# Optimization experiments

Hardware: AMD Instinct MI355X
Metric: run time of the kernel (lower is better)

Reference implementation:

```python
import jax, jax.numpy as jnp
import numpy as np

TOP_K = 2


def setup_inputs() -> dict:
    key = jax.random.key(0)
    ks = jax.random.split(key, 5)
    B, S, D, F, E = 2, 2048, 1024, 3584, 8
    scale_in = 1.0 / np.sqrt(D)
    scale_f = 1.0 / np.sqrt(F)
    return {
        "hidden_states": jax.random.normal(ks[0], (B, S, D), dtype=jnp.float32),
        "gate_w": jax.random.normal(ks[1], (E, D), dtype=jnp.float32) * scale_in,
        "w1": jax.random.normal(ks[2], (E, F, D), dtype=jnp.float32) * scale_in,
        "w3": jax.random.normal(ks[3], (E, F, D), dtype=jnp.float32) * scale_in,
        "w2": jax.random.normal(ks[4], (E, D, F), dtype=jnp.float32) * scale_f,
    }


def _routing_weights(logits):
    # softmax over experts, select top-k, renormalize (Mixtral semantics)
    probs = jax.nn.softmax(logits, axis=-1)          # [T, E]
    topv, topi = jax.lax.top_k(probs, TOP_K)          # [T, k]
    topv = topv / jnp.sum(topv, axis=-1, keepdims=True)
    T, E = logits.shape
    w = jnp.zeros((T, E), dtype=logits.dtype)
    w = w.at[jnp.arange(T)[:, None], topi].set(topv)  # dense [T, E] routing weights
    return w


def reference(hidden_states, gate_w, w1, w3, w2):
    B, S, D = hidden_states.shape
    x = hidden_states.reshape(-1, D)                  # [T, D]
    logits = x @ gate_w.T                             # [T, E]
    rw = _routing_weights(logits)                     # [T, E]
    E = gate_w.shape[0]
    out = jnp.zeros_like(x)
    for e in range(E):                                # fixed small expert count
        h = jax.nn.silu(x @ w1[e].T) * (x @ w3[e].T)  # [T, F]
        out = out + rw[:, e:e + 1] * (h @ w2[e].T)    # [T, D]
    return out.reshape(B, S, D)
```

## Files before the change

kernel.cpp:

```cpp
#include <hip/hip_runtime.h>
#include <hip/hip_bf16.h>


#define T_TOK 4096
#define DIM   1024
#define FF    3584
#define NE    8
#define CAP   (T_TOK*2 + NE*256)

#define OFF_TOPI   256UL
#define OFF_TOPW   33024UL
#define OFF_ROWTOK 65792UL
#define OFF_ROWW   106752UL
#define OFF_W1B    147712UL
#define OFF_W3B    (OFF_W1B + 58720256UL)
#define OFF_W2B    OFF_W1B
#define OFF_H      (OFF_W1B + 117440512UL)
#define WS_NEED    (OFF_H + 73400320UL)

using f32x4 = __attribute__((ext_vector_type(4))) float;
using s16x8 = __attribute__((ext_vector_type(8))) short;

__device__ __forceinline__ ushort f2b(float f) {
    __hip_bfloat16 b = __float2bfloat16(f);
    ushort u; __builtin_memcpy(&u, &b, 2); return u;
}
__device__ __forceinline__ void gl_lds16(const ushort* g, ushort* l) {
    __builtin_amdgcn_global_load_lds(
        (const __attribute__((address_space(1))) void*)g,
        (__attribute__((address_space(3))) void*)l, 16, 0, 0);
}
__device__ __forceinline__ uint4 pack8(float4 v0, float4 v1) {
    uint4 o;
    o.x = f2b(v0.x) | ((uint)f2b(v0.y) << 16);
    o.y = f2b(v0.z) | ((uint)f2b(v0.w) << 16);
    o.z = f2b(v1.x) | ((uint)f2b(v1.y) << 16);
    o.w = f2b(v1.z) | ((uint)f2b(v1.w) << 16);
    return o;
}

#define LGKM0 do { asm volatile("s_waitcnt lgkmcnt(0)" ::: "memory"); \
                   __builtin_amdgcn_sched_barrier(0); } while (0)
#define VMC(n) asm volatile("s_waitcnt vmcnt(" #n ")" ::: "memory")
#define BAR()  __builtin_amdgcn_s_barrier()

__global__ __launch_bounds__(256)
void k_route(const float* __restrict__ x, const float* __restrict__ gw,
             int* __restrict__ topi, float* __restrict__ topw,
             int* __restrict__ counts, ushort* __restrict__ xb)
{
    __shared__ float gws[NE*DIM];
    const int tid = threadIdx.x;
    for (int i = tid; i < NE*DIM/4; i += 256)
        ((float4*)gws)[i] = ((const float4*)gw)[i];
    __syncthreads();

    const int lane = tid & 63, wid = tid >> 6;
    const int t = blockIdx.x*4 + wid;

    float4 xr[4];
    const float4* xrow = (const float4*)(x + (size_t)t*DIM) + lane*4;
    #pragma unroll
    for (int i = 0; i < 4; ++i) xr[i] = xrow[i];

    uint4* xbd = (uint4*)(xb + (size_t)t*DIM);
    xbd[lane*2]   = pack8(xr[0], xr[1]);
    xbd[lane*2+1] = pack8(xr[2], xr[3]);

    float lg[NE];
    #pragma unroll
    for (int e = 0; e < NE; ++e) {
        const float4* g4 = (const float4*)(gws + e*DIM) + lane*4;
        float s = 0.f;
        #pragma unroll
        for (int i = 0; i < 4; ++i) {
            float4 g = g4[i];
            s += xr[i].x*g.x + xr[i].y*g.y + xr[i].z*g.z + xr[i].w*g.w;
        }
        #pragma unroll
        for (int off = 32; off; off >>= 1) s += __shfl_xor(s, off);
        lg[e] = s;
    }
    if (lane == 0) {
        float b1 = -1e30f, b2 = -1e30f; int i1 = 0, i2 = 0;
        #pragma unroll
        for (int e = 0; e < NE; ++e) {
            float v = lg[e];
            if (v > b1)      { b2 = b1; i2 = i1; b1 = v; i1 = e; }
            else if (v > b2) { b2 = v; i2 = e; }
        }
        float p2 = __expf(b2 - b1);
        float inv = 1.f / (1.f + p2);
        topi[2*t]   = i1; topi[2*t+1] = i2;
        topw[2*t]   = inv; topw[2*t+1] = p2*inv;
        atomicAdd(&counts[i1], 1); atomicAdd(&counts[i2], 1);
    }
}

__global__ void k_scan(const int* __restrict__ counts, int* __restrict__ offs,
                       int* __restrict__ rowTok)
{
    if (threadIdx.x == 0) {
        int acc = 0; offs[0] = 0;
        for (int e = 0; e < NE; ++e) {
            int p = (counts[e] + 255) & ~255;
            acc += p; offs[e+1] = acc;
        }
    }
    for (int i = threadIdx.x; i < CAP; i += blockDim.x) rowTok[i] = -1;
}

__global__ __launch_bounds__(256)
void k_scatter(const int* __restrict__ topi, const float* __restrict__ topw,
               const int* __restrict__ offs, int* __restrict__ cursor,
               int* __restrict__ rowTok, float* __restrict__ rowW)
{
    int t = blockIdx.x*256 + threadIdx.x;
    #pragma unroll
    for (int j = 0; j < 2; ++j) {
        int e = topi[2*t + j];
        int pos = offs[e] + atomicAdd(&cursor[e], 1);
        rowTok[pos] = t;
        rowW[pos] = topw[2*t + j];
    }
}

__global__ __launch_bounds__(256)
void k_cvt(const float* __restrict__ src, ushort* __restrict__ dst)
{
    size_t i = (size_t)blockIdx.x*256 + threadIdx.x;
    float4 v0 = ((const float4*)src)[2*i], v1 = ((const float4*)src)[2*i+1];
    ((uint4*)dst)[i] = pack8(v0, v1);
}

#define CVT_HALF ((NE*FF*DIM/8)/256)
__global__ __launch_bounds__(256)
void k_cvt2(const float* __restrict__ w1, const float* __restrict__ w3,
            ushort* __restrict__ w1b, ushort* __restrict__ w3b)
{
    int b = blockIdx.x;
    const float* src; ushort* dst;
    if (b < CVT_HALF) { src = w1; dst = w1b; }
    else              { src = w3; dst = w3b; b -= CVT_HALF; }
    size_t i = (size_t)b*256 + threadIdx.x;
    float4 v0 = ((const float4*)src)[2*i], v1 = ((const float4*)src)[2*i+1];
    ((uint4*)dst)[i] = pack8(v0, v1);
}

#define G1_SLOT 12288
__global__ __launch_bounds__(256, 2)
void k_gemm1(const ushort* __restrict__ xb,
             const ushort* __restrict__ w1b, const ushort* __restrict__ w3b,
             const int* __restrict__ offs, const int* __restrict__ rowTok,
             ushort* __restrict__ hout)
{
    __shared__ __align__(16) ushort L[3*G1_SLOT];
    const int sb = blockIdx.x;
    const int rowStart = blockIdx.y * 256;
    if (rowStart >= offs[8]) return;
    int e = 0;
    #pragma unroll
    for (int k = 1; k < NE; ++k) if (rowStart >= offs[k]) e = k;

    const int tid = threadIdx.x, lane = tid & 63, wid = tid >> 6;
    const int wr = wid >> 1, wc = wid & 1;
    const int lo = lane & 15, hi = lane >> 4;

    const int srow = lane >> 2;
    const int sch  = (lane & 3) ^ ((lane >> 3) & 3);
    const ushort* aS[4];
    #pragma unroll
    for (int j = 0; j < 4; ++j) {
        int tk = rowTok[rowStart + j*64 + wid*16 + srow]; if (tk < 0) tk = 0;
        aS[j] = xb + (size_t)tk*DIM + sch*8;
    }
    const ushort* bS[2];
    bS[0] = w1b + ((size_t)e*FF + sb*64 + wid*16 + srow)*DIM + sch*8;
    bS[1] = w3b + ((size_t)e*FF + sb*64 + wid*16 + srow)*DIM + sch*8;
    ushort* const dA = L + wid*512;
    ushort* const dB = L + 8192 + wid*512;

    const int sig = (lo >> 1) & 3;
    const int roff = ((hi ^ sig) * 8);
    int rdA[8], rdB[4];
    #pragma unroll
    for (int m = 0; m < 8; ++m) rdA[m] = (wr*128 + m*16 + lo)*32 + roff;
    #pragma unroll
    for (int n = 0; n < 2; ++n) {
        rdB[n]   = 8192 + (wc*32 + n*16 + lo)*32 + roff;
        rdB[n+2] = 8192 + (64 + wc*32 + n*16 + lo)*32 + roff;
    }

    f32x4 acc[8][4];
    #pragma unroll
    for (int m = 0; m < 8; ++m)
        #pragma unroll
        for (int n = 0; n < 4; ++n) acc[m][n] = (f32x4)(0.f);

    #pragma unroll
    for (int t0 = 0; t0 < 2; ++t0) {
        #pragma unroll
        for (int j = 0; j < 4; ++j) gl_lds16(aS[j] + t0*32, dA + t0*G1_SLOT + j*2048);
        #pragma unroll
        for (int j = 0; j < 2; ++j) gl_lds16(bS[j] + t0*32, dB + t0*G1_SLOT + j*2048);
    }
    VMC(6);
    BAR();

    const int NK = DIM/32;
    int cur = 0, nxt = 2;
    for (int t = 0; t < NK; ++t) {
        const ushort* Lb = L + cur*G1_SLOT;
        const bool pf = (t + 2 < NK);
        s16x8 a[4], b[4];
        #pragma unroll
        for (int n = 0; n < 4; ++n) b[n] = *(const s16x8*)(Lb + rdB[n]);
        #pragma unroll
        for (int m = 0; m < 4; ++m) a[m] = *(const s16x8*)(Lb + rdA[m]);
        if (pf) {
            #pragma unroll
            for (int j = 0; j < 3; ++j)
                gl_lds16(aS[j] + (t+2)*32, dA + nxt*G1_SLOT + j*2048);
        }
        BAR();
        LGKM0;
        __builtin_amdgcn_s_setprio(1);
        #pragma unroll
        for (int m = 0; m < 4; ++m)
            #pragma unroll
            for (int n = 0; n < 4; ++n)
                acc[m][n] = __builtin_amdgcn_mfma_f32_16x16x32_bf16(a[m], b[n], acc[m][n], 0, 0, 0);
        __builtin_amdgcn_s_setprio(0);
        BAR();
        #pragma unroll
        for (int m = 0; m < 4; ++m) a[m] = *(const s16x8*)(Lb + rdA[4+m]);
        if (pf) {
            gl_lds16(aS[3] + (t+2)*32, dA + nxt*G1_SLOT + 3*2048);
            gl_lds16(bS[0] + (t+2)*32, dB + nxt*G1_SLOT);
            gl_lds16(bS[1] + (t+2)*32, dB + nxt*G1_SLOT + 2048);
        }
        BAR();
        LGKM0;
        __builtin_amdgcn_s_setprio(1);
        #pragma unroll
        for (int m = 0; m < 4; ++m)
            #pragma unroll
            for (int n = 0; n < 4; ++n)
                acc[4+m][n] = __builtin_amdgcn_mfma_f32_16x16x32_bf16(a[m], b[n], acc[4+m][n], 0, 0, 0);
        __builtin_amdgcn_s_setprio(0);
        if (t < NK-2) { VMC(6); } else { VMC(0); }
        BAR();
        cur = (cur == 2) ? 0 : cur + 1;
        nxt = (nxt == 2) ? 0 : nxt + 1;
    }

    #pragma unroll
    for (int m = 0; m < 8; ++m)
        #pragma unroll
        for (int p = 0; p < 2; ++p) {
            f32x4 v1 = acc[m][p], v3 = acc[m][p+2];
            int f = sb*64 + wc*32 + p*16 + lo;
            #pragma unroll
            for (int j = 0; j < 4; ++j) {
                int row = rowStart + wr*128 + m*16 + hi*4 + j;
                float s = v1[j];
                float val = (s / (1.f + __expf(-s))) * v3[j];
                hout[(size_t)row*FF + f] = f2b(val);
            }
        }
}

__global__ __launch_bounds__(256, 2)
void k_gemm2(const ushort* __restrict__ h, const ushort* __restrict__ w2b,
             const int* __restrict__ offs, const int* __restrict__ rowTok,
             const float* __restrict__ rowW, float* __restrict__ out)
{
    __shared__ __align__(16) ushort L[3*G1_SLOT];
    const int dc = blockIdx.x * 128;
    const int rowStart = blockIdx.y * 256;
    if (rowStart >= offs[8]) return;
    int e = 0;
    #pragma unroll
    for (int k = 1; k < NE; ++k) if (rowStart >= offs[k]) e = k;
    const int kbase = blockIdx.z * (FF/4);

    const int tid = threadIdx.x, lane = tid & 63, wid = tid >> 6;
    const int wr = wid >> 1, wc = wid & 1;
    const int lo = lane & 15, hi = lane >> 4;

    const int srow = lane >> 2;
    const int sch  = (lane & 3) ^ ((lane >> 3) & 3);
    const ushort* aS[4];
    #pragma unroll
    for (int j = 0; j < 4; ++j)
        aS[j] = h + (size_t)(rowStart + j*64 + wid*16 + srow)*FF + kbase + sch*8;
    const ushort* bS[2];
    #pragma unroll
    for (int j = 0; j < 2; ++j)
        bS[j] = w2b + ((size_t)e*DIM + dc + j*64 + wid*16 + srow)*FF + kbase + sch*8;
    ushort* const dA = L + wid*512;
    ushort* const dB = L + 8192 + wid*512;

    const int sig = (lo >> 1) & 3;
    const int roff = ((hi ^ sig) * 8);
    int rdA[8], rdB[4];
    #pragma unroll
    for (int m = 0; m < 8; ++m) rdA[m] = (wr*128 + m*16 + lo)*32 + roff;
    #pragma unroll
    for (int n = 0; n < 4; ++n) rdB[n] = 8192 + (wc*64 + n*16 + lo)*32 + roff;

    f32x4 acc[8][4];
    #pragma unroll
    for (int m = 0; m < 8; ++m)
        #pragma unroll
        for (int n = 0; n < 4; ++n) acc[m][n] = (f32x4)(0.f);

    #pragma unroll
    for (int t0 = 0; t0 < 2; ++t0) {
        #pragma unroll
        for (int j = 0; j < 4; ++j) gl_lds16(aS[j] + t0*32, dA + t0*G1_SLOT + j*2048);
        #pragma unroll
        for (int j = 0; j < 2; ++j) gl_lds16(bS[j] + t0*32, dB + t0*G1_SLOT + j*2048);
    }
    VMC(6);
    BAR();

    const int NK = (FF/4)/32;
    int cur = 0, nxt = 2;
    for (int t = 0; t < NK; ++t) {
        const ushort* Lb = L + cur*G1_SLOT;
        const bool pf = (t + 2 < NK);
        s16x8 a[4], b[4];
        #pragma unroll
        for (int n = 0; n < 4; ++n) b[n] = *(const s16x8*)(Lb + rdB[n]);
        #pragma unroll
        for (int m = 0; m < 4; ++m) a[m] = *(const s16x8*)(Lb + rdA[m]);
        if (pf) {
            #pragma unroll
            for (int j = 0; j < 3; ++j)
                gl_lds16(aS[j] + (t+2)*32, dA + nxt*G1_SLOT + j*2048);
        }
        BAR();
        LGKM0;
        __builtin_amdgcn_s_setprio(1);
        #pragma unroll
        for (int m = 0; m < 4; ++m)
            #pragma unroll
            for (int n = 0; n < 4; ++n)
                acc[m][n] = __builtin_amdgcn_mfma_f32_16x16x32_bf16(a[m], b[n], acc[m][n], 0, 0, 0);
        __builtin_amdgcn_s_setprio(0);
        BAR();
        #pragma unroll
        for (int m = 0; m < 4; ++m) a[m] = *(const s16x8*)(Lb + rdA[4+m]);
        if (pf) {
            gl_lds16(aS[3] + (t+2)*32, dA + nxt*G1_SLOT + 3*2048);
            gl_lds16(bS[0] + (t+2)*32, dB + nxt*G1_SLOT);
            gl_lds16(bS[1] + (t+2)*32, dB + nxt*G1_SLOT + 2048);
        }
        BAR();
        LGKM0;
        __builtin_amdgcn_s_setprio(1);
        #pragma unroll
        for (int m = 0; m < 4; ++m)
            #pragma unroll
            for (int n = 0; n < 4; ++n)
                acc[4+m][n] = __builtin_amdgcn_mfma_f32_16x16x32_bf16(a[m], b[n], acc[4+m][n], 0, 0, 0);
        __builtin_amdgcn_s_setprio(0);
        if (t < NK-2) { VMC(6); } else { VMC(0); }
        BAR();
        cur = (cur == 2) ? 0 : cur + 1;
        nxt = (nxt == 2) ? 0 : nxt + 1;
    }

    #pragma unroll
    for (int m = 0; m < 8; ++m)
        #pragma unroll
        for (int j = 0; j < 4; ++j) {
            int prow = rowStart + wr*128 + m*16 + hi*4 + j;
            int tok = rowTok[prow];
            if (tok < 0) continue;
            float w = rowW[prow];
            #pragma unroll
            for (int n = 0; n < 4; ++n) {
                int d = dc + wc*64 + n*16 + lo;
                atomicAdd(&out[(size_t)tok*DIM + d], w * acc[m][n][j]);
            }
        }
}

extern "C" void kernel_launch(void* const* d_in, const int* in_sizes, int n_in,
                              void* d_out, int out_size, void* d_ws, size_t ws_size,
                              hipStream_t stream)
{
    const float* x  = (const float*)d_in[0];
    const float* gw = (const float*)d_in[1];
    const float* w1 = (const float*)d_in[2];
    const float* w3 = (const float*)d_in[3];
    const float* w2 = (const float*)d_in[4];
    float* out = (float*)d_out;
    char* ws = (char*)d_ws;
    if (ws_size < WS_NEED) return;

    int*    counts = (int*)ws;
    int*    cursor = counts + 8;
    int*    offs   = counts + 16;
    int*    topi   = (int*)  (ws + OFF_TOPI);
    float*  topw   = (float*)(ws + OFF_TOPW);
    int*    rowTok = (int*)  (ws + OFF_ROWTOK);
    float*  rowW   = (float*)(ws + OFF_ROWW);
    ushort* w1b    = (ushort*)(ws + OFF_W1B);
    ushort* w3b    = (ushort*)(ws + OFF_W3B);
    ushort* w2b    = (ushort*)(ws + OFF_W2B);
    ushort* h      = (ushort*)(ws + OFF_H);
    ushort* xb     = (ushort*)d_out;

    hipMemsetAsync(ws, 0, 256, stream);

    k_route  <<<T_TOK/4, 256, 0, stream>>>(x, gw, topi, topw, counts, xb);
    k_scan   <<<1, 256, 0, stream>>>(counts, offs, rowTok);
    k_scatter<<<T_TOK/256, 256, 0, stream>>>(topi, topw, offs, cursor, rowTok, rowW);
    k_cvt2   <<<2*CVT_HALF, 256, 0, stream>>>(w1, w3, w1b, w3b);
    k_gemm1  <<<dim3(56, CAP/256), 256, 0, stream>>>(xb, w1b, w3b, offs, rowTok, h);
    k_cvt    <<<(NE*DIM*FF/8)/256, 256, 0, stream>>>(w2, w2b);
    hipMemsetAsync(d_out, 0, (size_t)T_TOK*DIM*4, stream);
    k_gemm2  <<<dim3(8, CAP/256, 4), 256, 0, stream>>>(h, w2b, offs, rowTok, rowW, out);
}
```

Baseline: 557.0 us.

## Replace atomic scatter-add in down-projection with bf16 partials and gather combine

The second GEMM no longer scatters weighted fp32 results into the output with atomicAdd. Instead each of two K-split slices writes bf16 partial rows to a workspace buffer, and a new combine kernel gathers both expert rows per token, sums the slices, applies the routing weights and writes the output directly. The output memset is dropped and the K-split falls from four to two, giving fewer but longer blocks. This is meant to remove atomic contention and traffic, in exchange for an extra kernel, a partial-result round trip through memory, and bf16 rounding of the partials.

```diff
diff --git a/kernel.cpp b/kernel.cpp
--- a/kernel.cpp
+++ b/kernel.cpp
@@ -11,10 +11,11 @@
 #define OFF_TOPI   256UL
 #define OFF_TOPW   33024UL
 #define OFF_ROWTOK 65792UL
-#define OFF_ROWW   106752UL
+#define OFF_TOKPOS 106752UL
 #define OFF_W1B    147712UL
 #define OFF_W3B    (OFF_W1B + 58720256UL)
 #define OFF_W2B    OFF_W1B
+#define OFF_RES    OFF_W3B
 #define OFF_H      (OFF_W1B + 117440512UL)
 #define WS_NEED    (OFF_H + 73400320UL)
 
@@ -25,6 +26,8 @@
     __hip_bfloat16 b = __float2bfloat16(f);
     ushort u; __builtin_memcpy(&u, &b, 2); return u;
 }
+__device__ __forceinline__ float blo(uint u){ u <<= 16; float f; __builtin_memcpy(&f,&u,4); return f; }
+__device__ __forceinline__ float bhi(uint u){ u &= 0xFFFF0000u; float f; __builtin_memcpy(&f,&u,4); return f; }
 __device__ __forceinline__ void gl_lds16(const ushort* g, ushort* l) {
     __builtin_amdgcn_global_load_lds(
         (const __attribute__((address_space(1))) void*)g,
@@ -111,9 +114,9 @@
 }
 
 __global__ __launch_bounds__(256)
-void k_scatter(const int* __restrict__ topi, const float* __restrict__ topw,
+void k_scatter(const int* __restrict__ topi,
                const int* __restrict__ offs, int* __restrict__ cursor,
-               int* __restrict__ rowTok, float* __restrict__ rowW)
+               int* __restrict__ rowTok, int* __restrict__ tokPos)
 {
     int t = blockIdx.x*256 + threadIdx.x;
     #pragma unroll
@@ -121,7 +124,7 @@
         int e = topi[2*t + j];
         int pos = offs[e] + atomicAdd(&cursor[e], 1);
         rowTok[pos] = t;
-        rowW[pos] = topw[2*t + j];
+        tokPos[2*t + j] = pos;
     }
 }
 
@@ -272,8 +275,7 @@
 
 __global__ __launch_bounds__(256, 2)
 void k_gemm2(const ushort* __restrict__ h, const ushort* __restrict__ w2b,
-             const int* __restrict__ offs, const int* __restrict__ rowTok,
-             const float* __restrict__ rowW, float* __restrict__ out)
+             const int* __restrict__ offs, ushort* __restrict__ res)
 {
     __shared__ __align__(16) ushort L[3*G1_SLOT];
     const int dc = blockIdx.x * 128;
@@ -282,7 +284,7 @@
     int e = 0;
     #pragma unroll
     for (int k = 1; k < NE; ++k) if (rowStart >= offs[k]) e = k;
-    const int kbase = blockIdx.z * (FF/4);
+    const int kbase = blockIdx.z * (FF/2);
 
     const int tid = threadIdx.x, lane = tid & 63, wid = tid >> 6;
     const int wr = wid >> 1, wc = wid & 1;
@@ -325,7 +327,7 @@
     VMC(6);
     BAR();
 
-    const int NK = (FF/4)/32;
+    const int NK = (FF/2)/32;
     int cur = 0, nxt = 2;
     for (int t = 0; t < NK; ++t) {
         const ushort* Lb = L + cur*G1_SLOT;
@@ -372,20 +374,45 @@
         nxt = (nxt == 2) ? 0 : nxt + 1;
     }
 
+    ushort* rz = res + (size_t)blockIdx.z * CAP * DIM;
     #pragma unroll
     for (int m = 0; m < 8; ++m)
         #pragma unroll
         for (int j = 0; j < 4; ++j) {
             int prow = rowStart + wr*128 + m*16 + hi*4 + j;
-            int tok = rowTok[prow];
-            if (tok < 0) continue;
-            float w = rowW[prow];
             #pragma unroll
             for (int n = 0; n < 4; ++n) {
                 int d = dc + wc*64 + n*16 + lo;
-                atomicAdd(&out[(size_t)tok*DIM + d], w * acc[m][n][j]);
+                rz[(size_t)prow*DIM + d] = f2b(acc[m][n][j]);
             }
         }
+}
+
+__global__ __launch_bounds__(256)
+void k_combine(const ushort* __restrict__ res, const int* __restrict__ tokPos,
+               const float* __restrict__ topw, float* __restrict__ out)
+{
+    int i = blockIdx.x*256 + threadIdx.x;
+    int t = i >> 7;
+    int g = i & 127;
+    int pA = tokPos[2*t], pB = tokPos[2*t+1];
+    float wA = topw[2*t], wB = topw[2*t+1];
+    const ushort* res1 = res + (size_t)CAP * DIM;
+    uint4 a0 = *(const uint4*)(res  + (size_t)pA*DIM + g*8);
+    uint4 a1 = *(const uint4*)(res1 + (size_t)pA*DIM + g*8);
+    uint4 b0 = *(const uint4*)(res  + (size_t)pB*DIM + g*8);
+    uint4 b1 = *(const uint4*)(res1 + (size_t)pB*DIM + g*8);
+    float4 o0, o1;
+    o0.x = wA*(blo(a0.x)+blo(a1.x)) + wB*(blo(b0.x)+blo(b1.x));
+    o0.y = wA*(bhi(a0.x)+bhi(a1.x)) + wB*(bhi(b0.x)+bhi(b1.x));
+    o0.z = wA*(blo(a0.y)+blo(a1.y)) + wB*(blo(b0.y)+blo(b1.y));
+    o0.w = wA*(bhi(a0.y)+bhi(a1.y)) + wB*(bhi(b0.y)+bhi(b1.y));
+    o1.x = wA*(blo(a0.z)+blo(a1.z)) + wB*(blo(b0.z)+blo(b1.z));
+    o1.y = wA*(bhi(a0.z)+bhi(a1.z)) + wB*(bhi(b0.z)+bhi(b1.z));
+    o1.z = wA*(blo(a0.w)+blo(a1.w)) + wB*(blo(b0.w)+blo(b1.w));
+    o1.w = wA*(bhi(a0.w)+bhi(a1.w)) + wB*(bhi(b0.w)+bhi(b1.w));
+    float4* dst = (float4*)(out + (size_t)t*DIM + g*8);
+    dst[0] = o0; dst[1] = o1;
 }
 
 extern "C" void kernel_launch(void* const* d_in, const int* in_sizes, int n_in,
@@ -407,10 +434,11 @@
     int*    topi   = (int*)  (ws + OFF_TOPI);
     float*  topw   = (float*)(ws + OFF_TOPW);
     int*    rowTok = (int*)  (ws + OFF_ROWTOK);
-    float*  rowW   = (float*)(ws + OFF_ROWW);
+    int*    tokPos = (int*)  (ws + OFF_TOKPOS);
     ushort* w1b    = (ushort*)(ws + OFF_W1B);
     ushort* w3b    = (ushort*)(ws + OFF_W3B);
     ushort* w2b    = (ushort*)(ws + OFF_W2B);
+    ushort* res    = (ushort*)(ws + OFF_RES);
     ushort* h      = (ushort*)(ws + OFF_H);
     ushort* xb     = (ushort*)d_out;
 
@@ -418,10 +446,10 @@
 
     k_route  <<<T_TOK/4, 256, 0, stream>>>(x, gw, topi, topw, counts, xb);
     k_scan   <<<1, 256, 0, stream>>>(counts, offs, rowTok);
-    k_scatter<<<T_TOK/256, 256, 0, stream>>>(topi, topw, offs, cursor, rowTok, rowW);
+    k_scatter<<<T_TOK/256, 256, 0, stream>>>(topi, offs, cursor, rowTok, tokPos);
     k_cvt2   <<<2*CVT_HALF, 256, 0, stream>>>(w1, w3, w1b, w3b);
     k_gemm1  <<<dim3(56, CAP/256), 256, 0, stream>>>(xb, w1b, w3b, offs, rowTok, h);
     k_cvt    <<<(NE*DIM*FF/8)/256, 256, 0, stream>>>(w2, w2b);
-    hipMemsetAsync(d_out, 0, (size_t)T_TOK*DIM*4, stream);
-    k_gemm2  <<<dim3(8, CAP/256, 4), 256, 0, stream>>>(h, w2b, offs, rowTok, rowW, out);
-}
+    k_gemm2  <<<dim3(8, CAP/256, 2), 256, 0, stream>>>(h, w2b, offs, res);
+    k_combine<<<(T_TOK*DIM/8)/256, 256, 0, stream>>>(res, tokPos, topw, out);
+}
```

New measurement: 494.3 us. 11.2% less time.
